# Performance work log

Measured on AMD Instinct MI355X. Metric: run time of the kernel, lower is better.

Reference implementation:

```python
import jax, jax.numpy as jnp
import numpy as np

N = 100000
NODE_DIM = 128
HIDDEN_DIM = 64
E = 625000


def setup_inputs() -> dict:
    key = jax.random.key(0)
    k_x, k_e, k_w1, k_b1, k_w2, k_b2 = jax.random.split(key, 6)
    x = jax.random.normal(k_x, (N, NODE_DIM), dtype=jnp.float32)
    edge_index = jax.random.randint(k_e, (2, E), 0, N, dtype=jnp.int64)
    # nn.Linear default init: U(-1/sqrt(fan_in), 1/sqrt(fan_in))
    lim1 = 1.0 / np.sqrt(2 * NODE_DIM)
    W1 = jax.random.uniform(k_w1, (2 * NODE_DIM, HIDDEN_DIM), minval=-lim1, maxval=lim1, dtype=jnp.float32)
    b1 = jax.random.uniform(k_b1, (HIDDEN_DIM,), minval=-lim1, maxval=lim1, dtype=jnp.float32)
    lim2 = 1.0 / np.sqrt(HIDDEN_DIM)
    W2 = jax.random.uniform(k_w2, (HIDDEN_DIM, 1), minval=-lim2, maxval=lim2, dtype=jnp.float32)
    b2 = jax.random.uniform(k_b2, (1,), minval=-lim2, maxval=lim2, dtype=jnp.float32)
    return {"x": x, "edge_index": edge_index, "W1": W1, "b1": b1, "W2": W2, "b2": b2}


def reference(x, edge_index, W1, b1, W2, b2):
    row, col = edge_index[0], edge_index[1]
    # (E, 2*node_dim) gathered edge features
    edge_attr = jnp.concatenate([x[row], x[col]], axis=-1)
    h = jax.nn.relu(edge_attr @ W1 + b1)           # (E, hidden)
    edge_mask = jax.nn.sigmoid(h @ W2 + b2)[:, 0]  # (E,)
    return edge_mask
```

## Files before the change

kernel.cpp:

```cpp
#include <hip/hip_runtime.h>
#include <hip/hip_bf16.h>

typedef unsigned short u16x8 __attribute__((ext_vector_type(8)));
typedef __bf16 bf16x8 __attribute__((ext_vector_type(8)));
typedef float f32x4 __attribute__((ext_vector_type(4)));

#define NODE_DIM 128
#define HID 64

__device__ __forceinline__ unsigned short f2bf(float f) {
  union { float f; unsigned int u; } v; v.f = f;
  unsigned int u = v.u;
  u += 0x7fffu + ((u >> 16) & 1u);
  return (unsigned short)(u >> 16);
}
__device__ __forceinline__ float bf2f(unsigned short s) {
  union { unsigned int u; float f; } v; v.u = ((unsigned int)s) << 16;
  return v.f;
}

__global__ void prep_wt(const float* __restrict__ W1, unsigned short* __restrict__ Wt) {
  for (int i = blockIdx.x * blockDim.x + threadIdx.x; i < 128 * 128;
       i += gridDim.x * blockDim.x) {
    int j = i >> 7, k = i & 127;
    float w = (j < 64) ? W1[k * 64 + j] : W1[(k + 128) * 64 + (j - 64)];
    Wt[i] = f2bf(w);
  }
}

__global__ __launch_bounds__(256) void gemm_pq(const float* __restrict__ x,
                                               const unsigned short* __restrict__ Wt,
                                               unsigned short* __restrict__ PQ,
                                               int n_nodes) {
  __shared__ unsigned short xs[64][136];
  __shared__ unsigned short bs[128][136];
  const int tid = threadIdx.x;
  const int row0 = blockIdx.x * 64;

  for (int i = tid; i < 128 * 16; i += 256) {
    int j = i >> 4, c = i & 15;
    *(u16x8*)&bs[j][c * 8] = *(const u16x8*)&Wt[j * 128 + c * 8];
  }
  for (int i = tid; i < 64 * 32; i += 256) {
    int r = i >> 5, c = i & 31;
    int gr = row0 + r;
    float4 v = make_float4(0.f, 0.f, 0.f, 0.f);
    if (gr < n_nodes) v = *(const float4*)&x[(size_t)gr * NODE_DIM + c * 4];
    xs[r][c * 4 + 0] = f2bf(v.x); xs[r][c * 4 + 1] = f2bf(v.y);
    xs[r][c * 4 + 2] = f2bf(v.z); xs[r][c * 4 + 3] = f2bf(v.w);
  }
  __syncthreads();

  const int wave = tid >> 6, lane = tid & 63;
  const int m = lane & 15, q = lane >> 4;
  const int wrow = wave * 16;

  f32x4 acc[8];
  #pragma unroll
  for (int t = 0; t < 8; t++) acc[t] = f32x4{0.f, 0.f, 0.f, 0.f};

  #pragma unroll
  for (int kk = 0; kk < 4; kk++) {
    const int k0 = kk * 32;
    bf16x8 a = __builtin_bit_cast(bf16x8, *(const u16x8*)&xs[wrow + m][k0 + q * 8]);
    #pragma unroll
    for (int t = 0; t < 8; t++) {
      bf16x8 b = __builtin_bit_cast(bf16x8, *(const u16x8*)&bs[t * 16 + m][k0 + q * 8]);
      acc[t] = __builtin_amdgcn_mfma_f32_16x16x32_bf16(a, b, acc[t], 0, 0, 0);
    }
  }

  #pragma unroll
  for (int t = 0; t < 8; t++) {
    #pragma unroll
    for (int r = 0; r < 4; r++) {
      int gr = row0 + wrow + q * 4 + r;
      if (gr < n_nodes) PQ[(size_t)gr * 128 + t * 16 + m] = f2bf(acc[t][r]);
    }
  }
}

__global__ __launch_bounds__(256) void edge_mlp(const int* __restrict__ ei,
                                                const unsigned short* __restrict__ PQ,
                                                const float* __restrict__ b1,
                                                const float* __restrict__ W2,
                                                const float* __restrict__ b2,
                                                float* __restrict__ out, int E) {
  const int t = blockIdx.x * blockDim.x + threadIdx.x;
  const int l = t & 7;
  float w2r[8], b1r[8];
  #pragma unroll
  for (int i = 0; i < 8; i++) { w2r[i] = W2[l * 8 + i]; b1r[i] = b1[l * 8 + i]; }
  const float bias2 = b2[0];
  const int ngroups = (gridDim.x * blockDim.x) >> 3;
  for (int e = t >> 3; e < E; e += ngroups) {
    int row = ei[e];
    int col = ei[E + e];
    u16x8 pu = *(const u16x8*)&PQ[(size_t)row * 128 + l * 8];
    u16x8 qu = *(const u16x8*)&PQ[(size_t)col * 128 + 64 + l * 8];
    float partial = 0.f;
    #pragma unroll
    for (int i = 0; i < 8; i++) {
      float h = bf2f(pu[i]) + bf2f(qu[i]) + b1r[i];
      h = fmaxf(h, 0.f);
      partial = fmaf(h, w2r[i], partial);
    }
    partial += __shfl_xor(partial, 1);
    partial += __shfl_xor(partial, 2);
    partial += __shfl_xor(partial, 4);
    if (l == 0) out[e] = 1.f / (1.f + __expf(-(partial + bias2)));
  }
}

extern "C" void kernel_launch(void* const* d_in, const int* in_sizes, int n_in,
                              void* d_out, int out_size, void* d_ws, size_t ws_size,
                              hipStream_t stream) {
  const float* x  = (const float*)d_in[0];
  const int*   ei = (const int*)d_in[1];
  const float* W1 = (const float*)d_in[2];
  const float* b1 = (const float*)d_in[3];
  const float* W2 = (const float*)d_in[4];
  const float* b2 = (const float*)d_in[5];
  float* out = (float*)d_out;
  const int n_nodes = in_sizes[0] / NODE_DIM;
  const int E = in_sizes[1] / 2;

  unsigned short* Wt = (unsigned short*)d_ws;
  unsigned short* PQ = (unsigned short*)((char*)d_ws + 32768);

  prep_wt<<<16, 256, 0, stream>>>(W1, Wt);
  gemm_pq<<<(n_nodes + 63) / 64, 256, 0, stream>>>(x, Wt, PQ, n_nodes);
  edge_mlp<<<2048, 256, 0, stream>>>(ei, PQ, b1, W2, b2, out, E);
}
```

Baseline: 131.1 us.

## Drop LDS staging in node GEMM and use one edge per thread group

The node projection GEMM no longer stages x and the bf16 weights through shared memory. Each lane loads its A fragment straight from global memory into registers and converts it there, and reads the B fragments directly from the global weight buffer, which is small and cache-resident. This removes the LDS writes, the barrier and the 52 KB of shared memory per block, allowing higher occupancy at the cost of redundant global/L2 reads of the weights. The edge kernel switches from a grid-stride loop to a full grid with one 8-lane group per edge, trading per-thread register caching of b1/W2 for more parallelism and latency hiding on the gathers.

Result: slower. 145.3 us (+10.9%).

```diff
diff --git a/kernel.cpp b/kernel.cpp
--- a/kernel.cpp
+++ b/kernel.cpp
@@ -32,28 +32,20 @@
                                                const unsigned short* __restrict__ Wt,
                                                unsigned short* __restrict__ PQ,
                                                int n_nodes) {
-  __shared__ unsigned short xs[64][136];
-  __shared__ unsigned short bs[128][136];
   const int tid = threadIdx.x;
-  const int row0 = blockIdx.x * 64;
-
-  for (int i = tid; i < 128 * 16; i += 256) {
-    int j = i >> 4, c = i & 15;
-    *(u16x8*)&bs[j][c * 8] = *(const u16x8*)&Wt[j * 128 + c * 8];
-  }
-  for (int i = tid; i < 64 * 32; i += 256) {
-    int r = i >> 5, c = i & 31;
-    int gr = row0 + r;
-    float4 v = make_float4(0.f, 0.f, 0.f, 0.f);
-    if (gr < n_nodes) v = *(const float4*)&x[(size_t)gr * NODE_DIM + c * 4];
-    xs[r][c * 4 + 0] = f2bf(v.x); xs[r][c * 4 + 1] = f2bf(v.y);
-    xs[r][c * 4 + 2] = f2bf(v.z); xs[r][c * 4 + 3] = f2bf(v.w);
-  }
-  __syncthreads();
-
   const int wave = tid >> 6, lane = tid & 63;
   const int m = lane & 15, q = lane >> 4;
-  const int wrow = wave * 16;
+  const int row0 = blockIdx.x * 64 + wave * 16;
+
+  const int arow = min(row0 + m, n_nodes - 1);
+  const float* xr = x + (size_t)arow * NODE_DIM;
+
+  float4 av[4][2];
+  #pragma unroll
+  for (int kk = 0; kk < 4; kk++) {
+    av[kk][0] = *(const float4*)&xr[kk * 32 + q * 8];
+    av[kk][1] = *(const float4*)&xr[kk * 32 + q * 8 + 4];
+  }
 
   f32x4 acc[8];
   #pragma unroll
@@ -61,11 +53,16 @@
 
   #pragma unroll
   for (int kk = 0; kk < 4; kk++) {
-    const int k0 = kk * 32;
-    bf16x8 a = __builtin_bit_cast(bf16x8, *(const u16x8*)&xs[wrow + m][k0 + q * 8]);
+    union { unsigned short s[8]; u16x8 v; } au;
+    au.s[0] = f2bf(av[kk][0].x); au.s[1] = f2bf(av[kk][0].y);
+    au.s[2] = f2bf(av[kk][0].z); au.s[3] = f2bf(av[kk][0].w);
+    au.s[4] = f2bf(av[kk][1].x); au.s[5] = f2bf(av[kk][1].y);
+    au.s[6] = f2bf(av[kk][1].z); au.s[7] = f2bf(av[kk][1].w);
+    bf16x8 a = __builtin_bit_cast(bf16x8, au.v);
     #pragma unroll
     for (int t = 0; t < 8; t++) {
-      bf16x8 b = __builtin_bit_cast(bf16x8, *(const u16x8*)&bs[t * 16 + m][k0 + q * 8]);
+      bf16x8 b = __builtin_bit_cast(
+          bf16x8, *(const u16x8*)&Wt[(size_t)(t * 16 + m) * 128 + kk * 32 + q * 8]);
       acc[t] = __builtin_amdgcn_mfma_f32_16x16x32_bf16(a, b, acc[t], 0, 0, 0);
     }
   }
@@ -74,7 +71,7 @@
   for (int t = 0; t < 8; t++) {
     #pragma unroll
     for (int r = 0; r < 4; r++) {
-      int gr = row0 + wrow + q * 4 + r;
+      int gr = row0 + q * 4 + r;
       if (gr < n_nodes) PQ[(size_t)gr * 128 + t * 16 + m] = f2bf(acc[t][r]);
     }
   }
@@ -86,30 +83,24 @@
                                                 const float* __restrict__ W2,
                                                 const float* __restrict__ b2,
                                                 float* __restrict__ out, int E) {
-  const int t = blockIdx.x * blockDim.x + threadIdx.x;
-  const int l = t & 7;
-  float w2r[8], b1r[8];
+  const int t = blockIdx.x * 256 + threadIdx.x;
+  const int e = t >> 3, l = t & 7;
+  if (e >= E) return;
+  const int row = ei[e];
+  const int col = ei[E + e];
+  u16x8 pu = *(const u16x8*)&PQ[(size_t)row * 128 + l * 8];
+  u16x8 qu = *(const u16x8*)&PQ[(size_t)col * 128 + 64 + l * 8];
+  float partial = 0.f;
   #pragma unroll
-  for (int i = 0; i < 8; i++) { w2r[i] = W2[l * 8 + i]; b1r[i] = b1[l * 8 + i]; }
-  const float bias2 = b2[0];
-  const int ngroups = (gridDim.x * blockDim.x) >> 3;
-  for (int e = t >> 3; e < E; e += ngroups) {
-    int row = ei[e];
-    int col = ei[E + e];
-    u16x8 pu = *(const u16x8*)&PQ[(size_t)row * 128 + l * 8];
-    u16x8 qu = *(const u16x8*)&PQ[(size_t)col * 128 + 64 + l * 8];
-    float partial = 0.f;
-    #pragma unroll
-    for (int i = 0; i < 8; i++) {
-      float h = bf2f(pu[i]) + bf2f(qu[i]) + b1r[i];
-      h = fmaxf(h, 0.f);
-      partial = fmaf(h, w2r[i], partial);
-    }
-    partial += __shfl_xor(partial, 1);
-    partial += __shfl_xor(partial, 2);
-    partial += __shfl_xor(partial, 4);
-    if (l == 0) out[e] = 1.f / (1.f + __expf(-(partial + bias2)));
+  for (int i = 0; i < 8; i++) {
+    float h = bf2f(pu[i]) + bf2f(qu[i]) + b1[l * 8 + i];
+    h = fmaxf(h, 0.f);
+    partial = fmaf(h, W2[l * 8 + i], partial);
   }
+  partial += __shfl_xor(partial, 1);
+  partial += __shfl_xor(partial, 2);
+  partial += __shfl_xor(partial, 4);
+  if (l == 0) out[e] = 1.f / (1.f + __expf(-(partial + b2[0])));
 }
 
 extern "C" void kernel_launch(void* const* d_in, const int* in_sizes, int n_in,
@@ -130,5 +121,6 @@
 
   prep_wt<<<16, 256, 0, stream>>>(W1, Wt);
   gemm_pq<<<(n_nodes + 63) / 64, 256, 0, stream>>>(x, Wt, PQ, n_nodes);
-  edge_mlp<<<2048, 256, 0, stream>>>(ei, PQ, b1, W2, b2, out, E);
+  const int egrid = (E * 8 + 255) / 256;
+  edge_mlp<<<egrid, 256, 0, stream>>>(ei, PQ, b1, W2, b2, out, E);
 }
```
